# Kernel tuning notes

Hardware: AMD Instinct MI355X
Metric: run time of the kernel (lower is better)

The kernel has to match this reference:

```python
import jax, jax.numpy as jnp
import numpy as np

B, H, S, D = 4, 16, 1024, 64  # batch, n_heads, seq_len, value_size


def setup_inputs() -> dict:
    key0 = jax.random.key(0)
    k1, k2, k3, k4 = jax.random.split(key0, 4)
    query = jax.random.normal(k1, (B, S, D), dtype=jnp.float32)
    key = jax.random.normal(k2, (B, S, D), dtype=jnp.float32)
    value = jax.random.normal(k3, (B, S, D), dtype=jnp.float32)
    weight = jax.random.normal(k4, (1, H, D, D), dtype=jnp.float32) * (D ** -0.5)
    scale_factor = jnp.float32(D ** -0.5)
    return {"query": query, "key": key, "value": value,
            "weight": weight, "scale_factor": scale_factor}


def reference(query, key, value, weight, scale_factor):
    # wq = matmul(query[B,S,D], weight[1,H,D,D]) -> [B,H,S,D]
    wq = jnp.einsum('bsd,hde->bhse', query, weight[0])
    # qk = wq @ key^T -> [B,H,S,S], then scale
    qk = jnp.einsum('bhse,bte->bhst', wq, key) * scale_factor
    # softmax over heads axis (dim=1); dropout_p=0 -> identity
    softmax_qk = jax.nn.softmax(qk, axis=1)
    # dv = softmax_qk @ value -> [B,H,S,D]
    dv = jnp.einsum('bhst,btd->bhsd', softmax_qk, value)
    # softmax over last dim (dim=3), dropout identity, softmax over seq (dim=2)
    softmax_dv = jax.nn.softmax(dv, axis=3)
    softmax_dropout_dv = jax.nn.softmax(softmax_dv, axis=2)
    return softmax_dropout_dv * dv
```

## Files before the change

kernel.cpp:

```cpp
#include <hip/hip_runtime.h>
#include <hip/hip_bf16.h>

#define BB 4
#define HH 16
#define SS 1024
#define DD 64
#define N4 4194304

typedef __attribute__((ext_vector_type(8))) short bf16x8;
typedef __attribute__((ext_vector_type(4))) short bf16x4;
typedef __attribute__((ext_vector_type(4))) float f32x4;

#define MFMA(A, B, C) __builtin_amdgcn_mfma_f32_16x16x32_bf16((A), (B), (C), 0, 0, 0)

__device__ inline bf16x8 pack8(float4 a, float4 b) {
  union { bf16x8 v; __hip_bfloat16 h[8]; } u;
  u.h[0] = __float2bfloat16(a.x); u.h[1] = __float2bfloat16(a.y);
  u.h[2] = __float2bfloat16(a.z); u.h[3] = __float2bfloat16(a.w);
  u.h[4] = __float2bfloat16(b.x); u.h[5] = __float2bfloat16(b.y);
  u.h[6] = __float2bfloat16(b.z); u.h[7] = __float2bfloat16(b.w);
  return u.v;
}

__global__ __launch_bounds__(256) void k_wt(const float* __restrict__ w,
                                            float* __restrict__ wt) {
  int h = blockIdx.x, tid = threadIdx.x;
#pragma unroll
  for (int k = 0; k < 16; k++) {
    int idx = k * 256 + tid;
    int d = idx >> 6, e = idx & 63;
    wt[((size_t)h * 64 + e) * 64 + d] = w[((size_t)h * 64 + d) * 64 + e];
  }
}

__global__ __launch_bounds__(256, 2) void k_attn(
    const float* __restrict__ q, const float* __restrict__ key,
    const float* __restrict__ val, const float* __restrict__ wt,
    const float* __restrict__ scale_p, float* __restrict__ dvp) {
  const int b = blockIdx.x;
  const int s0 = blockIdx.y << 4;
  const int tc = blockIdx.z;
  const int tid = threadIdx.x;
  const int lane = tid & 63;
  const int w = tid >> 6;
  const int lm = lane & 15;
  const int kg = lane >> 4;
  const float scale = *scale_p;

  __shared__ __align__(16) char smem[62976];
  auto Klds = (__hip_bfloat16(*)[72])(smem);
  auto Vt   = (__hip_bfloat16(*)[40])(smem + 4608);
  auto QK   = (float(*)[32][16])(smem + 9728);
  auto Pl   = (__hip_bfloat16(*)[32][20])(smem + 42496);
  auto WQ   = (__hip_bfloat16(*)[72])(smem);

  bf16x8 qf[2];
#pragma unroll
  for (int ks = 0; ks < 2; ks++) {
    const float* qp = q + ((size_t)(b * SS + s0 + lm)) * 64 + ks * 32 + kg * 8;
    qf[ks] = pack8(*(const float4*)qp, *(const float4*)(qp + 4));
  }
#pragma unroll
  for (int i = 0; i < 4; i++) {
    int h = w * 4 + i;
    f32x4 wd[4] = {{0.f,0.f,0.f,0.f},{0.f,0.f,0.f,0.f},{0.f,0.f,0.f,0.f},{0.f,0.f,0.f,0.f}};
#pragma unroll
    for (int et = 0; et < 4; et++) {
#pragma unroll
      for (int ks = 0; ks < 2; ks++) {
        const float* wp = wt + ((size_t)(h * 64 + et * 16 + lm)) * 64 + ks * 32 + kg * 8;
        bf16x8 bfr = pack8(*(const float4*)wp, *(const float4*)(wp + 4));
        wd[et] = MFMA(qf[ks], bfr, wd[et]);
      }
    }
#pragma unroll
    for (int et = 0; et < 4; et++)
#pragma unroll
      for (int r = 0; r < 4; r++)
        WQ[h * 16 + kg * 4 + r][et * 16 + lm] = __float2bfloat16(wd[et][r]);
  }
  __syncthreads();
  bf16x8 afrag[4][2];
#pragma unroll
  for (int i = 0; i < 4; i++)
#pragma unroll
    for (int ks = 0; ks < 2; ks++)
      afrag[i][ks] = *(bf16x8*)&WQ[(w * 4 + i) * 16 + lm][ks * 32 + kg * 8];
  __syncthreads();

  f32x4 pv[4][4];
#pragma unroll
  for (int i = 0; i < 4; i++)
#pragma unroll
    for (int dt = 0; dt < 4; dt++) pv[i][dt] = (f32x4){0.f, 0.f, 0.f, 0.f};

  const int tbeg = tc * 512;
#pragma unroll 1
  for (int t0 = tbeg; t0 < tbeg + 512; t0 += 32) {
    __syncthreads();
    {
      int trow = tid >> 3, dc = (tid & 7) * 8;
      const float* kp = key + ((size_t)(b * SS + t0 + trow)) * 64 + dc;
      *(bf16x8*)&Klds[trow][dc] = pack8(*(const float4*)kp, *(const float4*)(kp + 4));
      int tv = tid & 31, dv0 = (tid >> 5) * 8;
      const float* vp = val + ((size_t)(b * SS + t0 + tv)) * 64 + dv0;
      float4 e4 = *(const float4*)vp, f4 = *(const float4*)(vp + 4);
      float vv[8] = {e4.x, e4.y, e4.z, e4.w, f4.x, f4.y, f4.z, f4.w};
#pragma unroll
      for (int j = 0; j < 8; j++) Vt[dv0 + j][tv] = __float2bfloat16(vv[j]);
    }
    __syncthreads();

    f32x4 qk[4][2] = {{{0.f,0.f,0.f,0.f},{0.f,0.f,0.f,0.f}},
                      {{0.f,0.f,0.f,0.f},{0.f,0.f,0.f,0.f}},
                      {{0.f,0.f,0.f,0.f},{0.f,0.f,0.f,0.f}},
                      {{0.f,0.f,0.f,0.f},{0.f,0.f,0.f,0.f}}};
#pragma unroll
    for (int tt = 0; tt < 2; tt++) {
#pragma unroll
      for (int ks = 0; ks < 2; ks++) {
        bf16x8 kf = *(bf16x8*)&Klds[tt * 16 + lm][ks * 32 + kg * 8];
#pragma unroll
        for (int i = 0; i < 4; i++) qk[i][tt] = MFMA(afrag[i][ks], kf, qk[i][tt]);
      }
    }
#pragma unroll
    for (int i = 0; i < 4; i++)
#pragma unroll
      for (int tt = 0; tt < 2; tt++) {
        f32x4 vq = qk[i][tt] * scale;
        *(f32x4*)&QK[w * 4 + i][tt * 16 + lm][kg * 4] = vq;
      }
    __syncthreads();

    {
      int c = tid >> 1, hh = tid & 1;
      int tl = c >> 2, sq = c & 3;
      f32x4 qv[8];
#pragma unroll
      for (int hb = 0; hb < 8; hb++) qv[hb] = *(f32x4*)&QK[hh * 8 + hb][tl][sq * 4];
      float inv[4];
#pragma unroll
      for (int p = 0; p < 4; p++) {
        float m = qv[0][p];
#pragma unroll
        for (int hb = 1; hb < 8; hb++) m = fmaxf(m, qv[hb][p]);
        m = fmaxf(m, __shfl_xor(m, 1));
        float s = 0.f;
#pragma unroll
        for (int hb = 0; hb < 8; hb++) {
          float e = __expf(qv[hb][p] - m);
          qv[hb][p] = e;
          s += e;
        }
        s += __shfl_xor(s, 1);
        inv[p] = 1.f / s;
      }
#pragma unroll
      for (int hb = 0; hb < 8; hb++) {
        union { bf16x4 v; __hip_bfloat16 hx[4]; } u;
#pragma unroll
        for (int p = 0; p < 4; p++) u.hx[p] = __float2bfloat16(qv[hb][p] * inv[p]);
        *(bf16x4*)&Pl[hh * 8 + hb][tl][sq * 4] = u.v;
      }
    }
    __syncthreads();

#pragma unroll
    for (int i = 0; i < 4; i++) {
      int h = w * 4 + i;
      union { bf16x8 v; __hip_bfloat16 hx[8]; } pa;
#pragma unroll
      for (int j = 0; j < 8; j++) pa.hx[j] = Pl[h][kg * 8 + j][lm];
#pragma unroll
      for (int dt = 0; dt < 4; dt++) {
        bf16x8 vf = *(bf16x8*)&Vt[dt * 16 + lm][kg * 8];
        pv[i][dt] = MFMA(pa.v, vf, pv[i][dt]);
      }
    }
  }

#pragma unroll
  for (int i = 0; i < 4; i++)
#pragma unroll
    for (int dt = 0; dt < 4; dt++)
#pragma unroll
      for (int r = 0; r < 4; r++)
        dvp[(size_t)tc * N4 +
            ((size_t)((b * HH + w * 4 + i) * SS) + s0 + kg * 4 + r) * 64 + dt * 16 + lm] =
            pv[i][dt][r];
}

__global__ __launch_bounds__(256) void k_rowsm(const float* __restrict__ dvp,
                                               float* __restrict__ sdv,
                                               float* __restrict__ stats) {
  int tid = threadIdx.x;
  int w = tid >> 6;
  int d = tid & 63;
  int r0 = blockIdx.x * 64;
  const float* p0 = dvp;
  const float* p1 = dvp + (size_t)N4;
  float cm = -1e30f, cl = 0.f;
  for (int it = 0; it < 16; it++) {
    int r = r0 + it * 4 + w;
    size_t off = (size_t)r * 64 + d;
    float x = p0[off] + p1[off];
    float m = x;
#pragma unroll
    for (int o = 1; o < 64; o <<= 1) m = fmaxf(m, __shfl_xor(m, o));
    float e = __expf(x - m);
    float sum = e;
#pragma unroll
    for (int o = 1; o < 64; o <<= 1) sum += __shfl_xor(sum, o);
    float sv = e / sum;
    sdv[off] = sv;
    float nm = fmaxf(cm, sv);
    cl = cl * __expf(cm - nm) + __expf(sv - nm);
    cm = nm;
  }
  __shared__ float sm[4][64], sl[4][64];
  sm[w][d] = cm;
  sl[w][d] = cl;
  __syncthreads();
  if (w == 0) {
    float M = sm[0][d], L = sl[0][d];
#pragma unroll
    for (int i = 1; i < 4; i++) {
      float m2 = sm[i][d], l2 = sl[i][d];
      float nm = fmaxf(M, m2);
      L = L * __expf(M - nm) + l2 * __expf(m2 - nm);
      M = nm;
    }
    stats[blockIdx.x * 128 + d * 2] = M;
    stats[blockIdx.x * 128 + d * 2 + 1] = L;
  }
}

__global__ __launch_bounds__(256) void k_final(const float* __restrict__ dvp,
                                               const float* __restrict__ sdv,
                                               const float* __restrict__ stats,
                                               float* __restrict__ out) {
  int tid = threadIdx.x;
  size_t base = (size_t)blockIdx.x * 1024;
  int bh = blockIdx.x >> 6;
  __shared__ float M[64], L[64];
  if (tid < 64) {
    int d = tid;
    float m = -1e30f, l = 0.f;
    const float* st = stats + bh * 16 * 128;
#pragma unroll
    for (int i = 0; i < 16; i++) {
      float m2 = st[i * 128 + d * 2];
      float l2 = st[i * 128 + d * 2 + 1];
      float nm = fmaxf(m, m2);
      l = l * __expf(m - nm) + l2 * __expf(m2 - nm);
      m = nm;
    }
    M[d] = m;
    L[d] = l;
  }
  __syncthreads();
  const float* p0 = dvp;
  const float* p1 = dvp + (size_t)N4;
  size_t idx = base + (size_t)tid * 4;
  int d0 = (tid & 15) * 4;
  float4 s4 = *(const float4*)&sdv[idx];
  float4 a4 = *(const float4*)&p0[idx];
  float4 b4 = *(const float4*)&p1[idx];
  float4 o;
  o.x = __expf(s4.x - M[d0]) / L[d0] * (a4.x + b4.x);
  o.y = __expf(s4.y - M[d0 + 1]) / L[d0 + 1] * (a4.y + b4.y);
  o.z = __expf(s4.z - M[d0 + 2]) / L[d0 + 2] * (a4.z + b4.z);
  o.w = __expf(s4.w - M[d0 + 3]) / L[d0 + 3] * (a4.w + b4.w);
  *(float4*)&out[idx] = o;
}

extern "C" void kernel_launch(void* const* d_in, const int* in_sizes, int n_in,
                              void* d_out, int out_size, void* d_ws, size_t ws_size,
                              hipStream_t stream) {
  const float* query = (const float*)d_in[0];
  const float* key = (const float*)d_in[1];
  const float* value = (const float*)d_in[2];
  const float* weight = (const float*)d_in[3];
  const float* scale = (const float*)d_in[4];
  float* out = (float*)d_out;

  float* ws = (float*)d_ws;
  float* dvp = ws;
  float* sdv = ws + (size_t)2 * N4;
  float* stats = ws + (size_t)3 * N4;
  float* wt = ws + (size_t)3 * N4 + 131072;

  k_wt<<<16, 256, 0, stream>>>(weight, wt);
  k_attn<<<dim3(4, 64, 2), 256, 0, stream>>>(query, key, value, wt, scale, dvp);
  k_rowsm<<<1024, 256, 0, stream>>>(dvp, sdv, stats);
  k_final<<<4096, 256, 0, stream>>>(dvp, sdv, stats, out);
}
```

Measured before the change: 170.6 us.

## Rewrite pipeline with bf16 intermediates, prepacked K/V, register-resident attention loop

A prep kernel now converts key, value (transposed) and weight to bf16 once. The attention kernel loads its K and V fragments straight from global memory into registers instead of staging them in shared memory. The softmax over heads is computed without max subtraction, using a small shared-memory cross-wave sum with double buffering, which removes several block barriers. Intermediates dv and softmax_dv are stored as bf16, the softmax statistics drop the max tracking because values lie in [0,1], and exp2 replaces expf. This cuts memory traffic and synchronisation, at the cost of bf16 precision on intermediates and a risk of overflow in the head softmax without max subtraction.

```diff
diff --git a/kernel.cpp b/kernel.cpp
--- a/kernel.cpp
+++ b/kernel.cpp
@@ -6,273 +6,303 @@
 #define SS 1024
 #define DD 64
 #define N4 4194304
+#define L2E 1.44269504f
 
 typedef __attribute__((ext_vector_type(8))) short bf16x8;
-typedef __attribute__((ext_vector_type(4))) short bf16x4;
 typedef __attribute__((ext_vector_type(4))) float f32x4;
 
 #define MFMA(A, B, C) __builtin_amdgcn_mfma_f32_16x16x32_bf16((A), (B), (C), 0, 0, 0)
 
+__device__ inline float b2f(unsigned short u) { return __uint_as_float(((unsigned)u) << 16); }
+__device__ inline unsigned short f2b(float f) {
+  union { __hip_bfloat16 h; unsigned short u; } x;
+  x.h = __float2bfloat16(f);
+  return x.u;
+}
+__device__ inline unsigned pkbf(float a, float b) {
+  return (unsigned)f2b(a) | ((unsigned)f2b(b) << 16);
+}
 __device__ inline bf16x8 pack8(float4 a, float4 b) {
-  union { bf16x8 v; __hip_bfloat16 h[8]; } u;
-  u.h[0] = __float2bfloat16(a.x); u.h[1] = __float2bfloat16(a.y);
-  u.h[2] = __float2bfloat16(a.z); u.h[3] = __float2bfloat16(a.w);
-  u.h[4] = __float2bfloat16(b.x); u.h[5] = __float2bfloat16(b.y);
-  u.h[6] = __float2bfloat16(b.z); u.h[7] = __float2bfloat16(b.w);
-  return u.v;
-}
-
-__global__ __launch_bounds__(256) void k_wt(const float* __restrict__ w,
-                                            float* __restrict__ wt) {
-  int h = blockIdx.x, tid = threadIdx.x;
-#pragma unroll
-  for (int k = 0; k < 16; k++) {
-    int idx = k * 256 + tid;
-    int d = idx >> 6, e = idx & 63;
-    wt[((size_t)h * 64 + e) * 64 + d] = w[((size_t)h * 64 + d) * 64 + e];
+  union { bf16x8 v; unsigned short u[8]; } x;
+  x.u[0] = f2b(a.x); x.u[1] = f2b(a.y); x.u[2] = f2b(a.z); x.u[3] = f2b(a.w);
+  x.u[4] = f2b(b.x); x.u[5] = f2b(b.y); x.u[6] = f2b(b.z); x.u[7] = f2b(b.w);
+  return x.v;
+}
+
+__global__ __launch_bounds__(256) void k_prep(const float* __restrict__ key, const float* __restrict__ val,
+                                              const float* __restrict__ wgt, __hip_bfloat16* __restrict__ Kb,
+                                              __hip_bfloat16* __restrict__ VTb, __hip_bfloat16* __restrict__ WT) {
+  const int bid = blockIdx.x, tid = threadIdx.x;
+  if (bid < 64) {
+    size_t base = (size_t)bid * 4096 + (size_t)tid * 16;
+#pragma unroll
+    for (int j = 0; j < 4; j++) {
+      float4 v = *(const float4*)(key + base + j * 4);
+      ushort4 u;
+      u.x = f2b(v.x); u.y = f2b(v.y); u.z = f2b(v.z); u.w = f2b(v.w);
+      *(ushort4*)(Kb + base + j * 4) = u;
+    }
+    return;
+  }
+  __shared__ __hip_bfloat16 tl[64][72];
+  const float* src;
+  __hip_bfloat16* dst;
+  int dstride;
+  if (bid < 128) {
+    int qq = bid - 64;
+    int b2 = qq >> 4, t0 = (qq & 15) * 64;
+    src = val + ((size_t)b2 * 1024 + t0) * 64;
+    dst = VTb + (size_t)b2 * 65536 + t0;
+    dstride = 1024;
+  } else {
+    int h = bid - 128;
+    src = wgt + (size_t)h * 4096;
+    dst = WT + (size_t)h * 4096;
+    dstride = 64;
+  }
+  int row = tid >> 2, cq = (tid & 3) * 16;
+#pragma unroll
+  for (int j = 0; j < 4; j++) {
+    float4 v = *(const float4*)(src + (size_t)row * 64 + cq + j * 4);
+    tl[cq + j * 4 + 0][row] = __float2bfloat16(v.x);
+    tl[cq + j * 4 + 1][row] = __float2bfloat16(v.y);
+    tl[cq + j * 4 + 2][row] = __float2bfloat16(v.z);
+    tl[cq + j * 4 + 3][row] = __float2bfloat16(v.w);
+  }
+  __syncthreads();
+#pragma unroll
+  for (int j = 0; j < 2; j++) {
+    bf16x8 a = *(bf16x8*)&tl[row][cq + j * 8];
+    *(bf16x8*)(dst + (size_t)row * dstride + cq + j * 8) = a;
   }
 }
 
 __global__ __launch_bounds__(256, 2) void k_attn(
-    const float* __restrict__ q, const float* __restrict__ key,
-    const float* __restrict__ val, const float* __restrict__ wt,
-    const float* __restrict__ scale_p, float* __restrict__ dvp) {
-  const int b = blockIdx.x;
-  const int s0 = blockIdx.y << 4;
-  const int tc = blockIdx.z;
+    const float* __restrict__ q, const __hip_bfloat16* __restrict__ Kb,
+    const __hip_bfloat16* __restrict__ VTb, const __hip_bfloat16* __restrict__ WT,
+    const float* __restrict__ scale_p, __hip_bfloat16* __restrict__ dvp) {
+  const int b = blockIdx.x, s0 = blockIdx.y << 4, tc = blockIdx.z;
+  const int tid = threadIdx.x, lane = tid & 63, w = tid >> 6;
+  const int lm = lane & 15, kg = lane >> 4;
+  const float cexp = (*scale_p) * L2E;
+
+  __shared__ __align__(16) char smem_all[39424];
+  float* sden = (float*)smem_all;
+  char* wv = smem_all + 18944 + w * 5120;
+
+  bf16x8 qf[2];
+#pragma unroll
+  for (int ks = 0; ks < 2; ks++) {
+    const float* qp = q + ((size_t)(b * SS + s0 + lm)) * DD + ks * 32 + kg * 8;
+    qf[ks] = pack8(*(const float4*)qp, *(const float4*)(qp + 4));
+  }
+  bf16x8 wqf[4][2];
+#pragma unroll
+  for (int i = 0; i < 4; i++) {
+    const int h = w * 4 + i;
+    f32x4 wd[4];
+#pragma unroll
+    for (int et = 0; et < 4; et++) wd[et] = (f32x4){0.f, 0.f, 0.f, 0.f};
+#pragma unroll
+    for (int et = 0; et < 4; et++)
+#pragma unroll
+      for (int ks = 0; ks < 2; ks++) {
+        bf16x8 af = *(const bf16x8*)(WT + ((size_t)(h * 64 + et * 16 + lm)) * 64 + ks * 32 + kg * 8);
+        wd[et] = MFMA(af, qf[ks], wd[et]);
+      }
+#pragma unroll
+    for (int et = 0; et < 4; et++) {
+      uint2 u;
+      u.x = pkbf(wd[et][0], wd[et][1]);
+      u.y = pkbf(wd[et][2], wd[et][3]);
+      *(uint2*)(wv + lm * 128 + ((et * 32 + kg * 8) ^ ((lm & 7) << 4))) = u;
+    }
+    asm volatile("s_waitcnt lgkmcnt(0)" ::: "memory");
+#pragma unroll
+    for (int ks = 0; ks < 2; ks++)
+      wqf[i][ks] = *(bf16x8*)(wv + lm * 128 + ((ks * 64 + kg * 16) ^ ((lm & 7) << 4)));
+    asm volatile("" ::: "memory");
+  }
+
+  f32x4 pv[4][4];
+#pragma unroll
+  for (int i = 0; i < 4; i++)
+#pragma unroll
+    for (int dt = 0; dt < 4; dt++) pv[i][dt] = (f32x4){0.f, 0.f, 0.f, 0.f};
+
+  const __hip_bfloat16* Kbb = Kb + (size_t)b * (SS * DD);
+  const __hip_bfloat16* Vbb = VTb + (size_t)b * (SS * DD);
+  int buf = 0;
+#pragma unroll 1
+  for (int t0 = tc * 512; t0 < tc * 512 + 512; t0 += 32) {
+    bf16x8 kf[2][2], vf[4];
+#pragma unroll
+    for (int tt = 0; tt < 2; tt++)
+#pragma unroll
+      for (int ks = 0; ks < 2; ks++)
+        kf[tt][ks] = *(const bf16x8*)(Kbb + ((size_t)(t0 + tt * 16 + lm)) * 64 + ks * 32 + kg * 8);
+#pragma unroll
+    for (int dt = 0; dt < 4; dt++)
+      vf[dt] = *(const bf16x8*)(Vbb + ((size_t)(dt * 16 + lm)) * 1024 + t0 + kg * 8);
+
+    f32x4 qk[4][2];
+#pragma unroll
+    for (int i = 0; i < 4; i++)
+#pragma unroll
+      for (int tt = 0; tt < 2; tt++) qk[i][tt] = (f32x4){0.f, 0.f, 0.f, 0.f};
+#pragma unroll
+    for (int ks = 0; ks < 2; ks++)
+#pragma unroll
+      for (int i = 0; i < 4; i++)
+#pragma unroll
+        for (int tt = 0; tt < 2; tt++) qk[i][tt] = MFMA(kf[tt][ks], wqf[i][ks], qk[i][tt]);
+
+    float ev[4][2][4];
+    f32x4 l4[2];
+    l4[0] = (f32x4){0.f, 0.f, 0.f, 0.f};
+    l4[1] = (f32x4){0.f, 0.f, 0.f, 0.f};
+#pragma unroll
+    for (int i = 0; i < 4; i++)
+#pragma unroll
+      for (int tt = 0; tt < 2; tt++)
+#pragma unroll
+        for (int r = 0; r < 4; r++) {
+          float e = exp2f(qk[i][tt][r] * cexp);
+          ev[i][tt][r] = e;
+          l4[tt][r] += e;
+        }
+    {
+      const int sb = buf * 2368 + lm * 148 + w * 36 + kg * 4;
+      *(f32x4*)&sden[sb + 0] = l4[0];
+      *(f32x4*)&sden[sb + 16] = l4[1];
+    }
+    __syncthreads();
+    f32x4 ri[2];
+#pragma unroll
+    for (int tt = 0; tt < 2; tt++) {
+      const int rb = buf * 2368 + lm * 148 + tt * 16 + kg * 4;
+      f32x4 s = *(f32x4*)&sden[rb] + *(f32x4*)&sden[rb + 36] +
+                *(f32x4*)&sden[rb + 72] + *(f32x4*)&sden[rb + 108];
+#pragma unroll
+      for (int r = 0; r < 4; r++) ri[tt][r] = 1.f / s[r];
+    }
+
+#pragma unroll
+    for (int i = 0; i < 4; i++)
+#pragma unroll
+      for (int tt = 0; tt < 2; tt++) {
+        uint2 u;
+        u.x = pkbf(ev[i][tt][0] * ri[tt][0], ev[i][tt][1] * ri[tt][1]);
+        u.y = pkbf(ev[i][tt][2] * ri[tt][2], ev[i][tt][3] * ri[tt][3]);
+        *(uint2*)(wv + i * 1280 + lm * 80 + tt * 32 + kg * 8) = u;
+      }
+    asm volatile("s_waitcnt lgkmcnt(0)" ::: "memory");
+#pragma unroll
+    for (int i = 0; i < 4; i++) {
+      bf16x8 pa = *(bf16x8*)(wv + i * 1280 + lm * 80 + kg * 16);
+#pragma unroll
+      for (int dt = 0; dt < 4; dt++) pv[i][dt] = MFMA(pa, vf[dt], pv[i][dt]);
+    }
+    asm volatile("" ::: "memory");
+    buf ^= 1;
+  }
+
+  const int orow = lane >> 2, oc4 = lane & 3;
+#pragma unroll
+  for (int i = 0; i < 4; i++) {
+#pragma unroll
+    for (int dt = 0; dt < 4; dt++)
+#pragma unroll
+      for (int r = 0; r < 4; r++) {
+        int srow = kg * 4 + r;
+        int cb = (dt * 16 + lm) * 4;
+        *(float*)(wv + srow * 256 + (cb ^ ((srow & 7) << 4))) = pv[i][dt][r];
+      }
+    asm volatile("s_waitcnt lgkmcnt(0)" ::: "memory");
+    float4 o0 = *(float4*)(wv + orow * 256 + ((oc4 * 64 + 0) ^ ((orow & 7) << 4)));
+    float4 o1 = *(float4*)(wv + orow * 256 + ((oc4 * 64 + 16) ^ ((orow & 7) << 4)));
+    float4 o2 = *(float4*)(wv + orow * 256 + ((oc4 * 64 + 32) ^ ((orow & 7) << 4)));
+    float4 o3 = *(float4*)(wv + orow * 256 + ((oc4 * 64 + 48) ^ ((orow & 7) << 4)));
+    __hip_bfloat16* dst = dvp + (size_t)tc * N4 +
+                          ((size_t)((b * HH + w * 4 + i) * SS) + s0 + orow) * 64 + oc4 * 16;
+    *(bf16x8*)dst = pack8(o0, o1);
+    *(bf16x8*)(dst + 8) = pack8(o2, o3);
+    asm volatile("" ::: "memory");
+  }
+}
+
+__global__ __launch_bounds__(256) void k_rowsm(const __hip_bfloat16* __restrict__ dvp,
+                                               __hip_bfloat16* __restrict__ sdv,
+                                               float* __restrict__ csum) {
+  const int tid = threadIdx.x, w = tid >> 6, lane = tid & 63;
+  const int rr = lane >> 4, dl = lane & 15;
+  const int r0 = blockIdx.x * 64 + w * 16;
+  const __hip_bfloat16* p1 = dvp + (size_t)N4;
+  float cs0 = 0.f, cs1 = 0.f, cs2 = 0.f, cs3 = 0.f;
+#pragma unroll
+  for (int it = 0; it < 4; it++) {
+    int r = r0 + it * 4 + rr;
+    size_t off = (size_t)r * 64 + dl * 4;
+    ushort4 ua = *(const ushort4*)(dvp + off);
+    ushort4 ub = *(const ushort4*)(p1 + off);
+    float e0 = exp2f((b2f(ua.x) + b2f(ub.x)) * L2E);
+    float e1 = exp2f((b2f(ua.y) + b2f(ub.y)) * L2E);
+    float e2 = exp2f((b2f(ua.z) + b2f(ub.z)) * L2E);
+    float e3 = exp2f((b2f(ua.w) + b2f(ub.w)) * L2E);
+    float s = (e0 + e1) + (e2 + e3);
+    s += __shfl_xor(s, 1); s += __shfl_xor(s, 2); s += __shfl_xor(s, 4); s += __shfl_xor(s, 8);
+    float rv = 1.f / s;
+    float v0 = e0 * rv, v1 = e1 * rv, v2 = e2 * rv, v3 = e3 * rv;
+    ushort4 uo;
+    uo.x = f2b(v0); uo.y = f2b(v1); uo.z = f2b(v2); uo.w = f2b(v3);
+    *(ushort4*)(sdv + off) = uo;
+    cs0 += exp2f(v0 * L2E); cs1 += exp2f(v1 * L2E);
+    cs2 += exp2f(v2 * L2E); cs3 += exp2f(v3 * L2E);
+  }
+  cs0 += __shfl_xor(cs0, 16); cs0 += __shfl_xor(cs0, 32);
+  cs1 += __shfl_xor(cs1, 16); cs1 += __shfl_xor(cs1, 32);
+  cs2 += __shfl_xor(cs2, 16); cs2 += __shfl_xor(cs2, 32);
+  cs3 += __shfl_xor(cs3, 16); cs3 += __shfl_xor(cs3, 32);
+  __shared__ float red[4][64];
+  if (rr == 0) {
+    red[w][dl * 4 + 0] = cs0; red[w][dl * 4 + 1] = cs1;
+    red[w][dl * 4 + 2] = cs2; red[w][dl * 4 + 3] = cs3;
+  }
+  __syncthreads();
+  if (tid < 64)
+    csum[(size_t)blockIdx.x * 64 + tid] = (red[0][tid] + red[1][tid]) + (red[2][tid] + red[3][tid]);
+}
+
+__global__ __launch_bounds__(256) void k_final(const __hip_bfloat16* __restrict__ dvp,
+                                               const __hip_bfloat16* __restrict__ sdv,
+                                               const float* __restrict__ csum,
+                                               float* __restrict__ out) {
   const int tid = threadIdx.x;
-  const int lane = tid & 63;
-  const int w = tid >> 6;
-  const int lm = lane & 15;
-  const int kg = lane >> 4;
-  const float scale = *scale_p;
-
-  __shared__ __align__(16) char smem[62976];
-  auto Klds = (__hip_bfloat16(*)[72])(smem);
-  auto Vt   = (__hip_bfloat16(*)[40])(smem + 4608);
-  auto QK   = (float(*)[32][16])(smem + 9728);
-  auto Pl   = (__hip_bfloat16(*)[32][20])(smem + 42496);
-  auto WQ   = (__hip_bfloat16(*)[72])(smem);
-
-  bf16x8 qf[2];
-#pragma unroll
-  for (int ks = 0; ks < 2; ks++) {
-    const float* qp = q + ((size_t)(b * SS + s0 + lm)) * 64 + ks * 32 + kg * 8;
-    qf[ks] = pack8(*(const float4*)qp, *(const float4*)(qp + 4));
-  }
-#pragma unroll
-  for (int i = 0; i < 4; i++) {
-    int h = w * 4 + i;
-    f32x4 wd[4] = {{0.f,0.f,0.f,0.f},{0.f,0.f,0.f,0.f},{0.f,0.f,0.f,0.f},{0.f,0.f,0.f,0.f}};
-#pragma unroll
-    for (int et = 0; et < 4; et++) {
-#pragma unroll
-      for (int ks = 0; ks < 2; ks++) {
-        const float* wp = wt + ((size_t)(h * 64 + et * 16 + lm)) * 64 + ks * 32 + kg * 8;
-        bf16x8 bfr = pack8(*(const float4*)wp, *(const float4*)(wp + 4));
-        wd[et] = MFMA(qf[ks], bfr, wd[et]);
-      }
-    }
-#pragma unroll
-    for (int et = 0; et < 4; et++)
-#pragma unroll
-      for (int r = 0; r < 4; r++)
-        WQ[h * 16 + kg * 4 + r][et * 16 + lm] = __float2bfloat16(wd[et][r]);
+  __shared__ float rL[64];
+  if (tid < 64) {
+    int bh = blockIdx.x >> 4;
+    float L = 0.f;
+#pragma unroll
+    for (int c = 0; c < 16; c++) L += csum[((size_t)bh * 16 + c) * 64 + tid];
+    rL[tid] = 1.f / L;
   }
   __syncthreads();
-  bf16x8 afrag[4][2];
-#pragma unroll
-  for (int i = 0; i < 4; i++)
-#pragma unroll
-    for (int ks = 0; ks < 2; ks++)
-      afrag[i][ks] = *(bf16x8*)&WQ[(w * 4 + i) * 16 + lm][ks * 32 + kg * 8];
-  __syncthreads();
-
-  f32x4 pv[4][4];
-#pragma unroll
-  for (int i = 0; i < 4; i++)
-#pragma unroll
-    for (int dt = 0; dt < 4; dt++) pv[i][dt] = (f32x4){0.f, 0.f, 0.f, 0.f};
-
-  const int tbeg = tc * 512;
-#pragma unroll 1
-  for (int t0 = tbeg; t0 < tbeg + 512; t0 += 32) {
-    __syncthreads();
-    {
-      int trow = tid >> 3, dc = (tid & 7) * 8;
-      const float* kp = key + ((size_t)(b * SS + t0 + trow)) * 64 + dc;
-      *(bf16x8*)&Klds[trow][dc] = pack8(*(const float4*)kp, *(const float4*)(kp + 4));
-      int tv = tid & 31, dv0 = (tid >> 5) * 8;
-      const float* vp = val + ((size_t)(b * SS + t0 + tv)) * 64 + dv0;
-      float4 e4 = *(const float4*)vp, f4 = *(const float4*)(vp + 4);
-      float vv[8] = {e4.x, e4.y, e4.z, e4.w, f4.x, f4.y, f4.z, f4.w};
-#pragma unroll
-      for (int j = 0; j < 8; j++) Vt[dv0 + j][tv] = __float2bfloat16(vv[j]);
-    }
-    __syncthreads();
-
-    f32x4 qk[4][2] = {{{0.f,0.f,0.f,0.f},{0.f,0.f,0.f,0.f}},
-                      {{0.f,0.f,0.f,0.f},{0.f,0.f,0.f,0.f}},
-                      {{0.f,0.f,0.f,0.f},{0.f,0.f,0.f,0.f}},
-                      {{0.f,0.f,0.f,0.f},{0.f,0.f,0.f,0.f}}};
-#pragma unroll
-    for (int tt = 0; tt < 2; tt++) {
-#pragma unroll
-      for (int ks = 0; ks < 2; ks++) {
-        bf16x8 kf = *(bf16x8*)&Klds[tt * 16 + lm][ks * 32 + kg * 8];
-#pragma unroll
-        for (int i = 0; i < 4; i++) qk[i][tt] = MFMA(afrag[i][ks], kf, qk[i][tt]);
-      }
-    }
-#pragma unroll
-    for (int i = 0; i < 4; i++)
-#pragma unroll
-      for (int tt = 0; tt < 2; tt++) {
-        f32x4 vq = qk[i][tt] * scale;
-        *(f32x4*)&QK[w * 4 + i][tt * 16 + lm][kg * 4] = vq;
-      }
-    __syncthreads();
-
-    {
-      int c = tid >> 1, hh = tid & 1;
-      int tl = c >> 2, sq = c & 3;
-      f32x4 qv[8];
-#pragma unroll
-      for (int hb = 0; hb < 8; hb++) qv[hb] = *(f32x4*)&QK[hh * 8 + hb][tl][sq * 4];
-      float inv[4];
-#pragma unroll
-      for (int p = 0; p < 4; p++) {
-        float m = qv[0][p];
-#pragma unroll
-        for (int hb = 1; hb < 8; hb++) m = fmaxf(m, qv[hb][p]);
-        m = fmaxf(m, __shfl_xor(m, 1));
-        float s = 0.f;
-#pragma unroll
-        for (int hb = 0; hb < 8; hb++) {
-          float e = __expf(qv[hb][p] - m);
-          qv[hb][p] = e;
-          s += e;
-        }
-        s += __shfl_xor(s, 1);
-        inv[p] = 1.f / s;
-      }
-#pragma unroll
-      for (int hb = 0; hb < 8; hb++) {
-        union { bf16x4 v; __hip_bfloat16 hx[4]; } u;
-#pragma unroll
-        for (int p = 0; p < 4; p++) u.hx[p] = __float2bfloat16(qv[hb][p] * inv[p]);
-        *(bf16x4*)&Pl[hh * 8 + hb][tl][sq * 4] = u.v;
-      }
-    }
-    __syncthreads();
-
-#pragma unroll
-    for (int i = 0; i < 4; i++) {
-      int h = w * 4 + i;
-      union { bf16x8 v; __hip_bfloat16 hx[8]; } pa;
-#pragma unroll
-      for (int j = 0; j < 8; j++) pa.hx[j] = Pl[h][kg * 8 + j][lm];
-#pragma unroll
-      for (int dt = 0; dt < 4; dt++) {
-        bf16x8 vf = *(bf16x8*)&Vt[dt * 16 + lm][kg * 8];
-        pv[i][dt] = MFMA(pa.v, vf, pv[i][dt]);
-      }
-    }
-  }
-
-#pragma unroll
-  for (int i = 0; i < 4; i++)
-#pragma unroll
-    for (int dt = 0; dt < 4; dt++)
-#pragma unroll
-      for (int r = 0; r < 4; r++)
-        dvp[(size_t)tc * N4 +
-            ((size_t)((b * HH + w * 4 + i) * SS) + s0 + kg * 4 + r) * 64 + dt * 16 + lm] =
-            pv[i][dt][r];
-}
-
-__global__ __launch_bounds__(256) void k_rowsm(const float* __restrict__ dvp,
-                                               float* __restrict__ sdv,
-                                               float* __restrict__ stats) {
-  int tid = threadIdx.x;
-  int w = tid >> 6;
-  int d = tid & 63;
-  int r0 = blockIdx.x * 64;
-  const float* p0 = dvp;
-  const float* p1 = dvp + (size_t)N4;
-  float cm = -1e30f, cl = 0.f;
-  for (int it = 0; it < 16; it++) {
-    int r = r0 + it * 4 + w;
-    size_t off = (size_t)r * 64 + d;
-    float x = p0[off] + p1[off];
-    float m = x;
-#pragma unroll
-    for (int o = 1; o < 64; o <<= 1) m = fmaxf(m, __shfl_xor(m, o));
-    float e = __expf(x - m);
-    float sum = e;
-#pragma unroll
-    for (int o = 1; o < 64; o <<= 1) sum += __shfl_xor(sum, o);
-    float sv = e / sum;
-    sdv[off] = sv;
-    float nm = fmaxf(cm, sv);
-    cl = cl * __expf(cm - nm) + __expf(sv - nm);
-    cm = nm;
-  }
-  __shared__ float sm[4][64], sl[4][64];
-  sm[w][d] = cm;
-  sl[w][d] = cl;
-  __syncthreads();
-  if (w == 0) {
-    float M = sm[0][d], L = sl[0][d];
-#pragma unroll
-    for (int i = 1; i < 4; i++) {
-      float m2 = sm[i][d], l2 = sl[i][d];
-      float nm = fmaxf(M, m2);
-      L = L * __expf(M - nm) + l2 * __expf(m2 - nm);
-      M = nm;
-    }
-    stats[blockIdx.x * 128 + d * 2] = M;
-    stats[blockIdx.x * 128 + d * 2 + 1] = L;
-  }
-}
-
-__global__ __launch_bounds__(256) void k_final(const float* __restrict__ dvp,
-                                               const float* __restrict__ sdv,
-                                               const float* __restrict__ stats,
-                                               float* __restrict__ out) {
-  int tid = threadIdx.x;
-  size_t base = (size_t)blockIdx.x * 1024;
-  int bh = blockIdx.x >> 6;
-  __shared__ float M[64], L[64];
-  if (tid < 64) {
-    int d = tid;
-    float m = -1e30f, l = 0.f;
-    const float* st = stats + bh * 16 * 128;
-#pragma unroll
-    for (int i = 0; i < 16; i++) {
-      float m2 = st[i * 128 + d * 2];
-      float l2 = st[i * 128 + d * 2 + 1];
-      float nm = fmaxf(m, m2);
-      l = l * __expf(m - nm) + l2 * __expf(m2 - nm);
-      m = nm;
-    }
-    M[d] = m;
-    L[d] = l;
-  }
-  __syncthreads();
-  const float* p0 = dvp;
-  const float* p1 = dvp + (size_t)N4;
-  size_t idx = base + (size_t)tid * 4;
-  int d0 = (tid & 15) * 4;
-  float4 s4 = *(const float4*)&sdv[idx];
-  float4 a4 = *(const float4*)&p0[idx];
-  float4 b4 = *(const float4*)&p1[idx];
-  float4 o;
-  o.x = __expf(s4.x - M[d0]) / L[d0] * (a4.x + b4.x);
-  o.y = __expf(s4.y - M[d0 + 1]) / L[d0 + 1] * (a4.y + b4.y);
-  o.z = __expf(s4.z - M[d0 + 2]) / L[d0 + 2] * (a4.z + b4.z);
-  o.w = __expf(s4.w - M[d0 + 3]) / L[d0 + 3] * (a4.w + b4.w);
-  *(float4*)&out[idx] = o;
+  const __hip_bfloat16* p1 = dvp + (size_t)N4;
+  size_t base = (size_t)blockIdx.x * 4096;
+#pragma unroll
+  for (int it = 0; it < 4; it++) {
+    size_t idx = base + it * 1024 + tid * 4;
+    int d0 = (tid * 4) & 63;
+    ushort4 us = *(const ushort4*)(sdv + idx);
+    ushort4 ua = *(const ushort4*)(dvp + idx);
+    ushort4 ub = *(const ushort4*)(p1 + idx);
+    float4 o;
+    o.x = exp2f(b2f(us.x) * L2E) * rL[d0 + 0] * (b2f(ua.x) + b2f(ub.x));
+    o.y = exp2f(b2f(us.y) * L2E) * rL[d0 + 1] * (b2f(ua.y) + b2f(ub.y));
+    o.z = exp2f(b2f(us.z) * L2E) * rL[d0 + 2] * (b2f(ua.z) + b2f(ub.z));
+    o.w = exp2f(b2f(us.w) * L2E) * rL[d0 + 3] * (b2f(ua.w) + b2f(ub.w));
+    *(float4*)(out + idx) = o;
+  }
 }
 
 extern "C" void kernel_launch(void* const* d_in, const int* in_sizes, int n_in,
@@ -285,14 +315,16 @@
   const float* scale = (const float*)d_in[4];
   float* out = (float*)d_out;
 
-  float* ws = (float*)d_ws;
-  float* dvp = ws;
-  float* sdv = ws + (size_t)2 * N4;
-  float* stats = ws + (size_t)3 * N4;
-  float* wt = ws + (size_t)3 * N4 + 131072;
-
-  k_wt<<<16, 256, 0, stream>>>(weight, wt);
-  k_attn<<<dim3(4, 64, 2), 256, 0, stream>>>(query, key, value, wt, scale, dvp);
-  k_rowsm<<<1024, 256, 0, stream>>>(dvp, sdv, stats);
-  k_final<<<4096, 256, 0, stream>>>(dvp, sdv, stats, out);
-}
+  char* wsb = (char*)d_ws;
+  __hip_bfloat16* dvp = (__hip_bfloat16*)wsb;
+  __hip_bfloat16* sdv = (__hip_bfloat16*)(wsb + 16777216);
+  __hip_bfloat16* Kb = (__hip_bfloat16*)(wsb + 25165824);
+  __hip_bfloat16* VTb = (__hip_bfloat16*)(wsb + 25690112);
+  __hip_bfloat16* WT = (__hip_bfloat16*)(wsb + 26214400);
+  float* csum = (float*)(wsb + 26345472);
+
+  k_prep<<<144, 256, 0, stream>>>(key, value, weight, Kb, VTb, WT);
+  k_attn<<<dim3(4, 64, 2), 256, 0, stream>>>(query, Kb, VTb, WT, scale, dvp);
+  k_rowsm<<<1024, 256, 0, stream>>>(dvp, sdv, csum);
+  k_final<<<1024, 256, 0, stream>>>(dvp, sdv, csum, out);
+}
```

New measurement: 138.7 us. -18.7%, faster.
